# Performance work log

Hardware: AMD Instinct MI355X
Metric: run time of the kernel (lower is better)

The kernel has to match this reference:

```python
import jax, jax.numpy as jnp
import numpy as np

B, N, D, H = 2, 4096, 512, 8
HD = D // H


def setup_inputs() -> dict:
    key = jax.random.key(0)
    k1, k2, k3, k4, k5 = jax.random.split(key, 5)
    s = D ** -0.5  # init scale to keep activations sane
    return {
        "x": jax.random.normal(k1, (B, N, D), dtype=jnp.float32),
        "Wq": jax.random.normal(k2, (D, D), dtype=jnp.float32) * s,
        "bq": jax.random.normal(k3, (D,), dtype=jnp.float32) * 0.01,
        "Wk": jax.random.normal(k4, (D, D), dtype=jnp.float32) * s,
        "bk": jax.random.normal(k5, (D,), dtype=jnp.float32) * 0.01,
    }


def reference(x, Wq, bq, Wk, bk):
    b, n, d = x.shape
    # Linear layers: y = x @ W^T + b (torch convention: W is [out, in])
    q = (jnp.einsum("bnd,ed->bne", x, Wq) + bq).reshape(b, n, H, HD).transpose(0, 2, 1, 3)
    k = (jnp.einsum("bnd,ed->bne", x, Wk) + bk).reshape(b, n, H, HD).transpose(0, 2, 1, 3)
    # FAITHFUL BUG: original uses self.k(x) for v as well
    v = k
    # FAITHFUL QUIRK: scale by full dim D, not head_dim
    scale = d ** -0.5
    attn = jnp.einsum("bhqe,bhke->bhqk", q, k) * scale  # [B,H,N,N] materialized, as in original
    attn = jax.nn.softmax(attn, axis=-1)
    out = jnp.einsum("bhqk,bhke->bhqe", attn, v)  # [B,H,N,HD]
    return out.transpose(0, 2, 1, 3).reshape(b, n, d)
```

## Files before the change

### kernel.cpp

```cpp
#include <hip/hip_runtime.h>

#define B_  2
#define N_  4096
#define D_  512
#define H_  8
#define HD_ 64
#define SCL2 (0.04419417382415922f * 1.4426950408889634f)

typedef float  f32x4  __attribute__((ext_vector_type(4)));
typedef float  f32x16 __attribute__((ext_vector_type(16)));
typedef short  s16x8  __attribute__((ext_vector_type(8)));
typedef short  s16x4  __attribute__((ext_vector_type(4)));
typedef unsigned int u32x4 __attribute__((ext_vector_type(4)));

#define MFMA16(a,b,c) __builtin_amdgcn_mfma_f32_16x16x32_bf16((a),(b),(c),0,0,0)
#define MFMA32(a,b,c) __builtin_amdgcn_mfma_f32_32x32x16_bf16((a),(b),(c),0,0,0)

__device__ __forceinline__ unsigned bf16rtn(float x){
    unsigned u = __float_as_uint(x);
    return (u + 0x7FFFu + ((u >> 16) & 1u)) >> 16;
}
__device__ __forceinline__ float bf16tof(unsigned h){
    return __uint_as_float(h << 16);
}
__device__ __forceinline__ unsigned cvt_pk_bf16(float lo, float hi){
    unsigned r;
    asm("v_cvt_pk_bf16_f32 %0, %1, %2" : "=v"(r) : "v"(lo), "v"(hi));
    return r;
}
__device__ __forceinline__ void perm32swap(unsigned &a, unsigned &b){
    asm volatile("v_permlane32_swap_b32 %0, %1" : "+v"(a), "+v"(b));
}
__device__ __forceinline__ int ix16(int r, int c){
    return (r << 6) + ((((c >> 3) ^ (r & 7)) << 3) | (c & 7));
}
__device__ __forceinline__ int ixt(int r, int c){
    return (r << 6) + ((((c >> 3) ^ (r & 7) ^ ((r >> 3) & 7)) << 3) | (c & 7));
}

__global__ __launch_bounds__(256) void split_kernel(
    const float* __restrict__ x, const float* __restrict__ Wq, const float* __restrict__ Wk,
    short* __restrict__ xh, short* __restrict__ xl,
    short* __restrict__ wqh, short* __restrict__ wql,
    short* __restrict__ wkh, short* __restrict__ wkl)
{
    const int bid = blockIdx.x;
    const float* src; short* dh; short* dl; size_t base;
    if (bid < 2048)      { src = x;  dh = xh;  dl = xl;  base = (size_t)bid * 2048; }
    else if (bid < 2176) { src = Wq; dh = wqh; dl = wql; base = (size_t)(bid - 2048) * 2048; }
    else                 { src = Wk; dh = wkh; dl = wkl; base = (size_t)(bid - 2176) * 2048; }

    const size_t off = base + (size_t)threadIdx.x * 8;
    float4 a = *(const float4*)&src[off];
    float4 c = *(const float4*)&src[off + 4];
    float v[8] = {a.x,a.y,a.z,a.w, c.x,c.y,c.z,c.w};
    s16x8 oh, ol;
    #pragma unroll
    for (int j = 0; j < 8; ++j) {
        unsigned hh = bf16rtn(v[j]);
        float lo = v[j] - bf16tof(hh);
        unsigned ll = bf16rtn(lo);
        oh[j] = (short)hh; ol[j] = (short)ll;
    }
    *(s16x8*)&dh[off] = oh;
    *(s16x8*)&dl[off] = ol;
}

__global__ __launch_bounds__(256, 2) void proj_gemm(
    const short* __restrict__ xh, const short* __restrict__ xl,
    const short* __restrict__ wqh, const short* __restrict__ wql,
    const short* __restrict__ wkh, const short* __restrict__ wkl,
    const float* __restrict__ bq, const float* __restrict__ bk,
    float* __restrict__ Qout, short* __restrict__ Khi, short* __restrict__ Klo)
{
    __shared__ short Ah[8192], Al[8192], Bh[8192], Bl[8192];

    const short* gWh  = blockIdx.z ? wkh : wqh;
    const short* gWl  = blockIdx.z ? wkl : wql;
    const float* bias = blockIdx.z ? bk  : bq;

    const int m0 = blockIdx.x * 128;
    const int e0 = blockIdx.y * 128;
    const int tid = threadIdx.x;
    const int wave = tid >> 6, lane = tid & 63;
    const int lr = lane & 15, lg = lane >> 4;

    int srow[4], scol[4];
    #pragma unroll
    for (int s = 0; s < 4; ++s) {
        int slot = s * 256 + tid;
        srow[s] = slot >> 3;
        scol[s] = (slot & 7) << 3;
    }

    f32x4 acc[2][8] = {};
    s16x8 pah[4], pal[4], pbh[4], pbl[4];

    #pragma unroll
    for (int s = 0; s < 4; ++s) {
        size_t ao = (size_t)(m0 + srow[s]) * D_ + scol[s];
        size_t bo = (size_t)(e0 + srow[s]) * D_ + scol[s];
        pah[s] = *(const s16x8*)&xh[ao];  pal[s] = *(const s16x8*)&xl[ao];
        pbh[s] = *(const s16x8*)&gWh[bo]; pbl[s] = *(const s16x8*)&gWl[bo];
    }

    for (int kt = 0; kt < 8; ++kt) {
        if (kt) __syncthreads();
        #pragma unroll
        for (int s = 0; s < 4; ++s) {
            int d = ix16(srow[s], scol[s]);
            *(s16x8*)&Ah[d] = pah[s];  *(s16x8*)&Al[d] = pal[s];
            *(s16x8*)&Bh[d] = pbh[s];  *(s16x8*)&Bl[d] = pbl[s];
        }
        __syncthreads();
        if (kt < 7) {
            const int k0 = (kt + 1) * 64;
            #pragma unroll
            for (int s = 0; s < 4; ++s) {
                size_t ao = (size_t)(m0 + srow[s]) * D_ + k0 + scol[s];
                size_t bo = (size_t)(e0 + srow[s]) * D_ + k0 + scol[s];
                pah[s] = *(const s16x8*)&xh[ao];  pal[s] = *(const s16x8*)&xl[ao];
                pbh[s] = *(const s16x8*)&gWh[bo]; pbl[s] = *(const s16x8*)&gWl[bo];
            }
        }
        __builtin_amdgcn_s_setprio(1);
        #pragma unroll
        for (int ks = 0; ks < 2; ++ks) {
            s16x8 afh[2], afl[2];
            #pragma unroll
            for (int f = 0; f < 2; ++f) {
                int a = ix16(wave*32 + f*16 + lr, ks*32 + lg*8);
                afh[f] = *(const s16x8*)&Ah[a];
                afl[f] = *(const s16x8*)&Al[a];
            }
            #pragma unroll
            for (int t = 0; t < 8; ++t) {
                int bA = ix16(t*16 + lr, ks*32 + lg*8);
                s16x8 bfh = *(const s16x8*)&Bh[bA];
                s16x8 bfl = *(const s16x8*)&Bl[bA];
                #pragma unroll
                for (int f = 0; f < 2; ++f) {
                    acc[f][t] = MFMA16(afh[f], bfh, acc[f][t]);
                    acc[f][t] = MFMA16(afh[f], bfl, acc[f][t]);
                    acc[f][t] = MFMA16(afl[f], bfh, acc[f][t]);
                }
            }
        }
        __builtin_amdgcn_s_setprio(0);
    }

    float bb[8];
    #pragma unroll
    for (int t = 0; t < 8; ++t) bb[t] = bias[e0 + t*16 + lr];

    if (blockIdx.z == 0) {
        #pragma unroll
        for (int f = 0; f < 2; ++f)
            #pragma unroll
            for (int t = 0; t < 8; ++t)
                #pragma unroll
                for (int r = 0; r < 4; ++r) {
                    int row = m0 + wave*32 + f*16 + lg*4 + r;
                    Qout[(size_t)row * D_ + e0 + t*16 + lr] = acc[f][t][r] + bb[t];
                }
    } else {
        #pragma unroll
        for (int f = 0; f < 2; ++f)
            #pragma unroll
            for (int t = 0; t < 8; ++t)
                #pragma unroll
                for (int r = 0; r < 4; ++r) {
                    int row = m0 + wave*32 + f*16 + lg*4 + r;
                    float v = acc[f][t][r] + bb[t];
                    unsigned hh = bf16rtn(v);
                    float lo = v - bf16tof(hh);
                    unsigned ll = bf16rtn(lo);
                    size_t o = (size_t)row * D_ + e0 + t*16 + lr;
                    Khi[o] = (short)hh;
                    Klo[o] = (short)ll;
                }
    }
}

__global__ __launch_bounds__(256) void proj_kernel(
    const float* __restrict__ x,
    const float* __restrict__ Wq, const float* __restrict__ bq,
    const float* __restrict__ Wk, const float* __restrict__ bk,
    float* __restrict__ Qout, short* __restrict__ Khi, short* __restrict__ Klo)
{
    const float* W    = blockIdx.z ? Wk : Wq;
    const float* bias = blockIdx.z ? bk : bq;

    const int m0 = blockIdx.x * 128;
    const int e0 = blockIdx.y * 128;

    __shared__ float Xs[128][36];
    __shared__ float Ws[128 * 36];

    const int tid = threadIdx.x;
    const int tx = tid & 15, ty = tid >> 4;

    float acc[8][8] = {};

    for (int k0 = 0; k0 < D_; k0 += 32) {
        #pragma unroll
        for (int s = 0; s < 4; ++s) {
            int slot = s * 256 + tid;
            int r  = slot >> 3;
            int c4 = (slot & 7) << 2;
            *(float4*)&Xs[r][c4] = *(const float4*)&x[(size_t)(m0 + r) * D_ + k0 + c4];
            int wblk = ((c4 >> 2) ^ (r >> 3)) & 7;
            *(float4*)&Ws[r * 36 + wblk * 4] = *(const float4*)&W[(size_t)(e0 + r) * D_ + k0 + c4];
        }
        __syncthreads();
        #pragma unroll
        for (int k = 0; k < 32; k += 4) {
            float4 xa[8], wb[8];
            #pragma unroll
            for (int i = 0; i < 8; ++i) xa[i] = *(float4*)&Xs[ty*8+i][k];
            #pragma unroll
            for (int j = 0; j < 8; ++j) {
                int row = tx*8 + j;
                int blk = ((k >> 2) ^ (row >> 3)) & 7;
                wb[j] = *(float4*)&Ws[row * 36 + blk * 4];
            }
            #pragma unroll
            for (int i = 0; i < 8; ++i)
                #pragma unroll
                for (int j = 0; j < 8; ++j)
                    acc[i][j] += xa[i].x*wb[j].x + xa[i].y*wb[j].y
                               + xa[i].z*wb[j].z + xa[i].w*wb[j].w;
        }
        __syncthreads();
    }

    const float4 bv0 = *(const float4*)&bias[e0 + tx*8];
    const float4 bv1 = *(const float4*)&bias[e0 + tx*8 + 4];
    const float bj[8] = {bv0.x,bv0.y,bv0.z,bv0.w, bv1.x,bv1.y,bv1.z,bv1.w};

    if (blockIdx.z == 0) {
        #pragma unroll
        for (int i = 0; i < 8; ++i) {
            float o[8];
            #pragma unroll
            for (int j = 0; j < 8; ++j) o[j] = acc[i][j] + bj[j];
            size_t off = (size_t)(m0 + ty*8 + i) * D_ + e0 + tx*8;
            *(float4*)&Qout[off]     = *(float4*)&o[0];
            *(float4*)&Qout[off + 4] = *(float4*)&o[4];
        }
    } else {
        #pragma unroll
        for (int i = 0; i < 8; ++i) {
            s16x8 oh, ol;
            #pragma unroll
            for (int j = 0; j < 8; ++j) {
                float v = acc[i][j] + bj[j];
                unsigned hh = bf16rtn(v);
                float lo = v - bf16tof(hh);
                unsigned ll = bf16rtn(lo);
                oh[j] = (short)hh; ol[j] = (short)ll;
            }
            size_t off = (size_t)(m0 + ty*8 + i) * D_ + e0 + tx*8;
            *(s16x8*)&Khi[off] = oh;
            *(s16x8*)&Klo[off] = ol;
        }
    }
}

__global__ __launch_bounds__(256, 2) void attn_kernel(
    const float* __restrict__ Q,
    const short* __restrict__ Khi, const short* __restrict__ Klo,
    float* __restrict__ out)
{
    __shared__ __align__(16) char smem[32768];
    short* Khs  = (short*)smem;
    short* Kls  = Khs + 4096;
    short* Kths = Kls + 4096;
    short* Ktls = Kths + 4096;

    const int bid = blockIdx.x;
    const int xcd = bid & 7, kk = bid >> 3;
    const int bh  = (xcd << 1) | (kk >> 5);
    const int qt  = kk & 31;
    const int b = bh >> 3, h = bh & 7;
    const int q0 = qt * 128;

    const int tid  = threadIdx.x;
    const int wave = tid >> 6, lane = tid & 63;
    const int lq   = lane & 31;
    const int hi   = lane >> 5;

    s16x8 qbh[4], qbl[4];
    {
        const int qrow = q0 + wave*32 + lq;
        const float* qp = Q + ((size_t)(b*N_ + qrow)) * D_ + h*HD_ + hi*8;
        #pragma unroll
        for (int s = 0; s < 4; ++s) {
            float4 a = *(const float4*)(qp + s*16);
            float4 c = *(const float4*)(qp + s*16 + 4);
            float v[8] = {a.x,a.y,a.z,a.w,c.x,c.y,c.z,c.w};
            #pragma unroll
            for (int j = 0; j < 8; ++j) {
                float xv = v[j] * SCL2;
                unsigned hh = bf16rtn(xv);
                float lo = xv - bf16tof(hh);
                qbh[s][j] = (short)hh;
                qbl[s][j] = (short)bf16rtn(lo);
            }
        }
    }

    f32x16 oacc[2] = {};
    float mrun = -1e30f, lrun = 0.f;

    const int br = tid >> 4, bc = tid & 15;
    s16x4 rh[4], rl[4];

    {
        const size_t kbase = ((size_t)(b*N_ + br*4)) * D_ + h*HD_ + bc*4;
        #pragma unroll
        for (int i = 0; i < 4; ++i) {
            rh[i] = *(const s16x4*)&Khi[kbase + (size_t)i * D_];
            rl[i] = *(const s16x4*)&Klo[kbase + (size_t)i * D_];
        }
    }

    for (int kt = 0; kt < 64; ++kt) {
        #pragma unroll
        for (int i = 0; i < 4; ++i) {
            *(s16x4*)&Khs[ix16(br*4+i, bc*4)] = rh[i];
            *(s16x4*)&Kls[ix16(br*4+i, bc*4)] = rl[i];
        }
        #pragma unroll
        for (int j = 0; j < 4; ++j) {
            s16x4 th = { rh[0][j], rh[1][j], rh[2][j], rh[3][j] };
            s16x4 tl = { rl[0][j], rl[1][j], rl[2][j], rl[3][j] };
            *(s16x4*)&Kths[ixt(bc*4+j, br*4)] = th;
            *(s16x4*)&Ktls[ixt(bc*4+j, br*4)] = tl;
        }
        __syncthreads();

        if (kt < 63) {
            const size_t kbase = ((size_t)(b*N_ + (kt+1)*64 + br*4)) * D_ + h*HD_ + bc*4;
            #pragma unroll
            for (int i = 0; i < 4; ++i) {
                rh[i] = *(const s16x4*)&Khi[kbase + (size_t)i * D_];
                rl[i] = *(const s16x4*)&Klo[kbase + (size_t)i * D_];
            }
        }

        f32x16 sacc[2] = {};
        __builtin_amdgcn_s_setprio(1);
        #pragma unroll
        for (int t = 0; t < 2; ++t) {
            #pragma unroll
            for (int s = 0; s < 4; ++s) {
                s16x8 ah = *(const s16x8*)&Khs[ix16(t*32 + lq, s*16 + hi*8)];
                s16x8 al = *(const s16x8*)&Kls[ix16(t*32 + lq, s*16 + hi*8)];
                sacc[t] = MFMA32(ah, qbh[s], sacc[t]);
                sacc[t] = MFMA32(ah, qbl[s], sacc[t]);
                sacc[t] = MFMA32(al, qbh[s], sacc[t]);
            }
        }
        __builtin_amdgcn_s_setprio(0);

        float tr[16];
        #pragma unroll
        for (int r = 0; r < 16; ++r) tr[r] = fmaxf(sacc[0][r], sacc[1][r]);
        #pragma unroll
        for (int st = 8; st >= 1; st >>= 1)
            #pragma unroll
            for (int r = 0; r < st; ++r) tr[r] = fmaxf(tr[r], tr[r + st]);
        float mt = fmaxf(tr[0], __shfl_xor(tr[0], 32));
        const float mn  = fmaxf(mrun, mt);
        const float al_ = __builtin_amdgcn_exp2f(mrun - mn);
        mrun = mn;

        f32x16 p[2];
        #pragma unroll
        for (int t = 0; t < 2; ++t)
            #pragma unroll
            for (int r = 0; r < 16; ++r)
                p[t][r] = __builtin_amdgcn_exp2f(sacc[t][r] - mn);
        #pragma unroll
        for (int r = 0; r < 16; ++r) tr[r] = p[0][r] + p[1][r];
        #pragma unroll
        for (int st = 8; st >= 1; st >>= 1)
            #pragma unroll
            for (int r = 0; r < st; ++r) tr[r] += tr[r + st];
        float rs = tr[0] + __shfl_xor(tr[0], 32);
        lrun = lrun * al_ + rs;
        #pragma unroll
        for (int dt = 0; dt < 2; ++dt)
            #pragma unroll
            for (int r = 0; r < 16; ++r)
                oacc[dt][r] *= al_;

        __builtin_amdgcn_s_setprio(1);
        #pragma unroll
        for (int s = 0; s < 4; ++s) {
            const int tt = s >> 1, r0 = (s & 1) * 8;
            float ph[8], pl[8];
            #pragma unroll
            for (int j = 0; j < 8; ++j) {
                float pv = p[tt][r0 + j];
                float hf = __uint_as_float(__float_as_uint(pv) & 0xFFFF0000u);
                ph[j] = hf;
                pl[j] = pv - hf;
            }
            unsigned h0 = cvt_pk_bf16(ph[0], ph[1]);
            unsigned h1 = cvt_pk_bf16(ph[4], ph[5]);
            perm32swap(h0, h1);
            unsigned h2 = cvt_pk_bf16(ph[2], ph[3]);
            unsigned h3 = cvt_pk_bf16(ph[6], ph[7]);
            perm32swap(h2, h3);
            u32x4 wph = { h0, h2, h1, h3 };
            s16x8 pfh = __builtin_bit_cast(s16x8, wph);

            unsigned l0 = cvt_pk_bf16(pl[0], pl[1]);
            unsigned l1 = cvt_pk_bf16(pl[4], pl[5]);
            perm32swap(l0, l1);
            unsigned l2 = cvt_pk_bf16(pl[2], pl[3]);
            unsigned l3 = cvt_pk_bf16(pl[6], pl[7]);
            perm32swap(l2, l3);
            u32x4 wpl = { l0, l2, l1, l3 };
            s16x8 pfl = __builtin_bit_cast(s16x8, wpl);

            #pragma unroll
            for (int dt = 0; dt < 2; ++dt) {
                s16x8 vh = *(const s16x8*)&Kths[ixt(dt*32 + lq, s*16 + hi*8)];
                s16x8 vl = *(const s16x8*)&Ktls[ixt(dt*32 + lq, s*16 + hi*8)];
                oacc[dt] = MFMA32(vh, pfh, oacc[dt]);
                oacc[dt] = MFMA32(vl, pfh, oacc[dt]);
                oacc[dt] = MFMA32(vh, pfl, oacc[dt]);
            }
        }
        __builtin_amdgcn_s_setprio(0);
        __syncthreads();
    }

    const float inv = 1.0f / lrun;
    float* Os = (float*)smem;
    #pragma unroll
    for (int dt = 0; dt < 2; ++dt)
        #pragma unroll
        for (int g = 0; g < 4; ++g) {
            f32x4 w;
            #pragma unroll
            for (int e = 0; e < 4; ++e)
                w[e] = oacc[dt][g*4 + e] * inv;
            const int q = wave*32 + lq;
            const int dbase = dt*32 + g*8 + hi*4;
            *(f32x4*)&Os[q*64 + (dbase ^ (q & 28))] = w;
        }
    __syncthreads();
    #pragma unroll
    for (int rep = 0; rep < 8; ++rep) {
        const int row = (tid >> 4) + rep*16;
        const int c4  = (tid & 15) * 4;
        f32x4 w = *(const f32x4*)&Os[row*64 + (c4 ^ (row & 28))];
        *(f32x4*)&out[((size_t)(b*N_ + q0 + row)) * D_ + h*HD_ + c4] = w;
    }
}

extern "C" void kernel_launch(void* const* d_in, const int* in_sizes, int n_in,
                              void* d_out, int out_size, void* d_ws, size_t ws_size,
                              hipStream_t stream)
{
    const float* x  = (const float*)d_in[0];
    const float* Wq = (const float*)d_in[1];
    const float* bq = (const float*)d_in[2];
    const float* Wk = (const float*)d_in[3];
    const float* bk = (const float*)d_in[4];
    float* outp = (float*)d_out;

    char* wsb = (char*)d_ws;
    float* Qw  = (float*)wsb;
    short* Khi = (short*)(wsb + 16777216);
    short* Klo = Khi + 4194304;

    if (ws_size >= 52428800) {
        short* xh  = (short*)(wsb + 33554432);
        short* xl  = xh + 4194304;
        short* wqh = (short*)(wsb + 50331648);
        short* wql = wqh + 262144;
        short* wkh = wql + 262144;
        short* wkl = wkh + 262144;

        split_kernel<<<dim3(2304), dim3(256), 0, stream>>>(
            x, Wq, Wk, xh, xl, wqh, wql, wkh, wkl);
        proj_gemm<<<dim3(64, 4, 2), dim3(256), 0, stream>>>(
            xh, xl, wqh, wql, wkh, wkl, bq, bk, Qw, Khi, Klo);
    } else {
        dim3 gp(64, 4, 2);
        proj_kernel<<<gp, dim3(256), 0, stream>>>(x, Wq, bq, Wk, bk, Qw, Khi, Klo);
    }

    attn_kernel<<<dim3(512), dim3(256), 0, stream>>>(Qw, Khi, Klo, outp);
}
```

Baseline: 317.7 us.

## Split attention KV range across blocks with merge kernel and lazy rescaling

Shrinks attention blocks to 128 threads over 64 query rows and splits the key range into two halves per query tile, so 2048 blocks run instead of 512. A new merge kernel then combines the partial outputs using their saved max and sum values. The online-softmax rescale is skipped unless the running max grows by more than 8 (log2 units), which removes per-tile multiplies on the output accumulators. The cost is writing and re-reading partial outputs through workspace plus an extra launch, and the workspace reuses the region that holds the split-x buffers.

Measured after the change: 384.9 us. +21.1%, slower.

```diff
diff --git a/kernel.cpp b/kernel.cpp
--- a/kernel.cpp
+++ b/kernel.cpp
@@ -267,10 +267,11 @@
     }
 }
 
-__global__ __launch_bounds__(256, 2) void attn_kernel(
+template<int SPLIT>
+__global__ __launch_bounds__(128, 4) void attn_kernel(
     const float* __restrict__ Q,
     const short* __restrict__ Khi, const short* __restrict__ Klo,
-    float* __restrict__ out)
+    float* __restrict__ out, float* __restrict__ Opart, float* __restrict__ Ml)
 {
     __shared__ __align__(16) char smem[32768];
     short* Khs  = (short*)smem;
@@ -279,11 +280,26 @@
     short* Ktls = Kths + 4096;
 
     const int bid = blockIdx.x;
-    const int xcd = bid & 7, kk = bid >> 3;
-    const int bh  = (xcd << 1) | (kk >> 5);
-    const int qt  = kk & 31;
+    const int xcd = bid & 7;
+    int bh, qt, ks, pidx;
+    if (SPLIT) {
+        const int idx = bid >> 3;
+        bh = (xcd << 1) | (idx >> 7);
+        const int rem = idx & 127;
+        qt = rem >> 1;
+        ks = rem & 1;
+        pidx = (bh * 64 + qt) * 2 + ks;
+    } else {
+        const int idx = bid >> 3;
+        bh = (xcd << 1) | (idx >> 6);
+        qt = idx & 63;
+        ks = 0;
+        pidx = 0;
+    }
     const int b = bh >> 3, h = bh & 7;
-    const int q0 = qt * 128;
+    const int q0 = qt * 64;
+    const int kt0 = SPLIT ? ks * 32 : 0;
+    const int nkt = SPLIT ? 32 : 64;
 
     const int tid  = threadIdx.x;
     const int wave = tid >> 6, lane = tid & 63;
@@ -314,36 +330,39 @@
     float mrun = -1e30f, lrun = 0.f;
 
     const int br = tid >> 4, bc = tid & 15;
-    s16x4 rh[4], rl[4];
+    s16x4 rh[8], rl[8];
 
     {
-        const size_t kbase = ((size_t)(b*N_ + br*4)) * D_ + h*HD_ + bc*4;
-        #pragma unroll
-        for (int i = 0; i < 4; ++i) {
+        const size_t kbase = ((size_t)(b*N_ + kt0*64 + br*8)) * D_ + h*HD_ + bc*4;
+        #pragma unroll
+        for (int i = 0; i < 8; ++i) {
             rh[i] = *(const s16x4*)&Khi[kbase + (size_t)i * D_];
             rl[i] = *(const s16x4*)&Klo[kbase + (size_t)i * D_];
         }
     }
 
-    for (int kt = 0; kt < 64; ++kt) {
-        #pragma unroll
-        for (int i = 0; i < 4; ++i) {
-            *(s16x4*)&Khs[ix16(br*4+i, bc*4)] = rh[i];
-            *(s16x4*)&Kls[ix16(br*4+i, bc*4)] = rl[i];
-        }
-        #pragma unroll
-        for (int j = 0; j < 4; ++j) {
-            s16x4 th = { rh[0][j], rh[1][j], rh[2][j], rh[3][j] };
-            s16x4 tl = { rl[0][j], rl[1][j], rl[2][j], rl[3][j] };
-            *(s16x4*)&Kths[ixt(bc*4+j, br*4)] = th;
-            *(s16x4*)&Ktls[ixt(bc*4+j, br*4)] = tl;
-        }
-        __syncthreads();
-
-        if (kt < 63) {
-            const size_t kbase = ((size_t)(b*N_ + (kt+1)*64 + br*4)) * D_ + h*HD_ + bc*4;
-            #pragma unroll
-            for (int i = 0; i < 4; ++i) {
+    for (int it = 0; it < nkt; ++it) {
+        const int kt = kt0 + it;
+        #pragma unroll
+        for (int i = 0; i < 8; ++i) {
+            *(s16x4*)&Khs[ix16(br*8+i, bc*4)] = rh[i];
+            *(s16x4*)&Kls[ix16(br*8+i, bc*4)] = rl[i];
+        }
+        #pragma unroll
+        for (int half = 0; half < 2; ++half)
+            #pragma unroll
+            for (int j = 0; j < 4; ++j) {
+                s16x4 th = { rh[half*4+0][j], rh[half*4+1][j], rh[half*4+2][j], rh[half*4+3][j] };
+                s16x4 tl = { rl[half*4+0][j], rl[half*4+1][j], rl[half*4+2][j], rl[half*4+3][j] };
+                *(s16x4*)&Kths[ixt(bc*4+j, br*8 + half*4)] = th;
+                *(s16x4*)&Ktls[ixt(bc*4+j, br*8 + half*4)] = tl;
+            }
+        __syncthreads();
+
+        if (it < nkt - 1) {
+            const size_t kbase = ((size_t)(b*N_ + (kt+1)*64 + br*8)) * D_ + h*HD_ + bc*4;
+            #pragma unroll
+            for (int i = 0; i < 8; ++i) {
                 rh[i] = *(const s16x4*)&Khi[kbase + (size_t)i * D_];
                 rl[i] = *(const s16x4*)&Klo[kbase + (size_t)i * D_];
             }
@@ -372,29 +391,31 @@
             #pragma unroll
             for (int r = 0; r < st; ++r) tr[r] = fmaxf(tr[r], tr[r + st]);
         float mt = fmaxf(tr[0], __shfl_xor(tr[0], 32));
-        const float mn  = fmaxf(mrun, mt);
-        const float al_ = __builtin_amdgcn_exp2f(mrun - mn);
-        mrun = mn;
+        if (__any(mt > mrun + 8.0f)) {
+            const float mn  = fmaxf(mrun, mt);
+            const float al_ = __builtin_amdgcn_exp2f(mrun - mn);
+            mrun = mn;
+            lrun *= al_;
+            #pragma unroll
+            for (int dt = 0; dt < 2; ++dt)
+                #pragma unroll
+                for (int r = 0; r < 16; ++r)
+                    oacc[dt][r] *= al_;
+        }
 
         f32x16 p[2];
         #pragma unroll
         for (int t = 0; t < 2; ++t)
             #pragma unroll
             for (int r = 0; r < 16; ++r)
-                p[t][r] = __builtin_amdgcn_exp2f(sacc[t][r] - mn);
+                p[t][r] = __builtin_amdgcn_exp2f(sacc[t][r] - mrun);
         #pragma unroll
         for (int r = 0; r < 16; ++r) tr[r] = p[0][r] + p[1][r];
         #pragma unroll
         for (int st = 8; st >= 1; st >>= 1)
             #pragma unroll
             for (int r = 0; r < st; ++r) tr[r] += tr[r + st];
-        float rs = tr[0] + __shfl_xor(tr[0], 32);
-        lrun = lrun * al_ + rs;
-        #pragma unroll
-        for (int dt = 0; dt < 2; ++dt)
-            #pragma unroll
-            for (int r = 0; r < 16; ++r)
-                oacc[dt][r] *= al_;
+        lrun += tr[0] + __shfl_xor(tr[0], 32);
 
         __builtin_amdgcn_s_setprio(1);
         #pragma unroll
@@ -439,27 +460,86 @@
         __syncthreads();
     }
 
-    const float inv = 1.0f / lrun;
-    float* Os = (float*)smem;
+    if (SPLIT) {
+        float* Op = Opart + (size_t)pidx * 4096;
+        #pragma unroll
+        for (int dt = 0; dt < 2; ++dt)
+            #pragma unroll
+            for (int r = 0; r < 16; ++r) {
+                const int d = dt*32 + (r & 3) + 8*(r >> 2) + 4*hi;
+                Op[d*64 + wave*32 + lq] = oacc[dt][r];
+            }
+        if (hi == 0) {
+            Ml[(size_t)pidx*128 + wave*32 + lq]      = mrun;
+            Ml[(size_t)pidx*128 + 64 + wave*32 + lq] = lrun;
+        }
+    } else {
+        const float inv = 1.0f / lrun;
+        float* Os = (float*)smem;
+        __syncthreads();
+        #pragma unroll
+        for (int dt = 0; dt < 2; ++dt)
+            #pragma unroll
+            for (int g = 0; g < 4; ++g) {
+                f32x4 w;
+                #pragma unroll
+                for (int e = 0; e < 4; ++e)
+                    w[e] = oacc[dt][g*4 + e] * inv;
+                const int q = wave*32 + lq;
+                const int dbase = dt*32 + g*8 + hi*4;
+                *(f32x4*)&Os[q*64 + (dbase ^ (q & 28))] = w;
+            }
+        __syncthreads();
+        #pragma unroll
+        for (int rep = 0; rep < 8; ++rep) {
+            const int row = (tid >> 4) + rep*8;
+            const int c4  = (tid & 15) * 4;
+            f32x4 w = *(const f32x4*)&Os[row*64 + (c4 ^ (row & 28))];
+            *(f32x4*)&out[((size_t)(b*N_ + q0 + row)) * D_ + h*HD_ + c4] = w;
+        }
+    }
+}
+
+__global__ __launch_bounds__(256) void merge_kernel(
+    const float* __restrict__ Opart, const float* __restrict__ Ml,
+    float* __restrict__ out)
+{
+    const int bid = blockIdx.x;
+    const int bh = bid >> 6, qt = bid & 63;
+    const int b = bh >> 3, h = bh & 7;
+    const int q0 = qt * 64;
+    const int p0 = bid * 2, p1 = bid * 2 + 1;
+
+    const int tid = threadIdx.x;
+    const int tq = tid & 63, dg = tid >> 6;
+
+    const float m1 = Ml[(size_t)p0*128 + tq], l1 = Ml[(size_t)p0*128 + 64 + tq];
+    const float m2 = Ml[(size_t)p1*128 + tq], l2 = Ml[(size_t)p1*128 + 64 + tq];
+    const float m  = fmaxf(m1, m2);
+    const float s1 = __builtin_amdgcn_exp2f(m1 - m);
+    const float s2 = __builtin_amdgcn_exp2f(m2 - m);
+    const float linv = 1.0f / (l1*s1 + l2*s2);
+
+    __shared__ float T[64 * 65];
+    const float* O1 = Opart + (size_t)p0 * 4096;
+    const float* O2 = Opart + (size_t)p1 * 4096;
     #pragma unroll
-    for (int dt = 0; dt < 2; ++dt)
-        #pragma unroll
-        for (int g = 0; g < 4; ++g) {
-            f32x4 w;
-            #pragma unroll
-            for (int e = 0; e < 4; ++e)
-                w[e] = oacc[dt][g*4 + e] * inv;
-            const int q = wave*32 + lq;
-            const int dbase = dt*32 + g*8 + hi*4;
-            *(f32x4*)&Os[q*64 + (dbase ^ (q & 28))] = w;
-        }
+    for (int i = 0; i < 16; ++i) {
+        const int d = dg*16 + i;
+        const float v = (O1[d*64 + tq]*s1 + O2[d*64 + tq]*s2) * linv;
+        T[tq*65 + d] = v;
+    }
     __syncthreads();
+
+    const int row = tid >> 2;
+    const int c0  = (tid & 3) * 16;
     #pragma unroll
-    for (int rep = 0; rep < 8; ++rep) {
-        const int row = (tid >> 4) + rep*16;
-        const int c4  = (tid & 15) * 4;
-        f32x4 w = *(const f32x4*)&Os[row*64 + (c4 ^ (row & 28))];
-        *(f32x4*)&out[((size_t)(b*N_ + q0 + row)) * D_ + h*HD_ + c4] = w;
+    for (int g = 0; g < 4; ++g) {
+        f32x4 w;
+        #pragma unroll
+        for (int e = 0; e < 4; ++e)
+            w[e] = T[row*65 + c0 + g*4 + e];
+        *(f32x4*)&out[((size_t)(b*N_ + q0 + row)) * D_ + h*HD_ + c0 + g*4] = w;
     }
 }
 
@@ -496,5 +576,14 @@
         proj_kernel<<<gp, dim3(256), 0, stream>>>(x, Wq, bq, Wk, bk, Qw, Khi, Klo);
     }
 
-    attn_kernel<<<dim3(512), dim3(256), 0, stream>>>(Qw, Khi, Klo, outp);
-}
+    if (ws_size >= 68157440) {
+        float* Opart = (float*)(wsb + 33554432);
+        float* Ml    = (float*)(wsb + 67108864);
+        attn_kernel<1><<<dim3(2048), dim3(128), 0, stream>>>(
+            Qw, Khi, Klo, outp, Opart, Ml);
+        merge_kernel<<<dim3(1024), dim3(256), 0, stream>>>(Opart, Ml, outp);
+    } else {
+        attn_kernel<0><<<dim3(1024), dim3(128), 0, stream>>>(
+            Qw, Khi, Klo, outp, nullptr, nullptr);
+    }
+}
```

## Double K tile to 128 rows and add lazy softmax rescaling

Applied to the files above, without the earlier changes.

The attention kernel now stages 128 keys per iteration instead of 64, which doubles shared memory to 64KB and halves the number of loop iterations and barriers. A new swizzle handles the wider transposed K tile. The online softmax now skips rescaling the running max, sum and output accumulator unless some lane's tile max exceeds the running max by more than 8 in log2 units. This trades fewer rescale multiplies for more registers per thread and the LDS occupancy limit implied by 64KB per block with launch_bounds(256,2).

After: 291.8 us. -8.1%, faster.

```diff
diff --git a/kernel.cpp b/kernel.cpp
--- a/kernel.cpp
+++ b/kernel.cpp
@@ -34,8 +34,8 @@
 __device__ __forceinline__ int ix16(int r, int c){
     return (r << 6) + ((((c >> 3) ^ (r & 7)) << 3) | (c & 7));
 }
-__device__ __forceinline__ int ixt(int r, int c){
-    return (r << 6) + ((((c >> 3) ^ (r & 7) ^ ((r >> 3) & 7)) << 3) | (c & 7));
+__device__ __forceinline__ int ixt2(int r, int c){
+    return (r << 7) + ((((c >> 3) ^ ((r >> 2) & 15)) << 3) | (c & 7));
 }
 
 __global__ __launch_bounds__(256) void split_kernel(
@@ -272,11 +272,11 @@
     const short* __restrict__ Khi, const short* __restrict__ Klo,
     float* __restrict__ out)
 {
-    __shared__ __align__(16) char smem[32768];
+    __shared__ __align__(16) char smem[65536];
     short* Khs  = (short*)smem;
-    short* Kls  = Khs + 4096;
-    short* Kths = Kls + 4096;
-    short* Ktls = Kths + 4096;
+    short* Kls  = Khs + 8192;
+    short* Kths = Kls + 8192;
+    short* Ktls = Kths + 8192;
 
     const int bid = blockIdx.x;
     const int xcd = bid & 7, kk = bid >> 3;
@@ -313,46 +313,47 @@
     f32x16 oacc[2] = {};
     float mrun = -1e30f, lrun = 0.f;
 
-    const int br = tid >> 4, bc = tid & 15;
-    s16x4 rh[4], rl[4];
+    const int rg = tid >> 4, bc = tid & 15;
+    s16x4 rh[8], rl[8];
 
     {
-        const size_t kbase = ((size_t)(b*N_ + br*4)) * D_ + h*HD_ + bc*4;
-        #pragma unroll
-        for (int i = 0; i < 4; ++i) {
+        const size_t kbase = ((size_t)(b*N_ + rg*8)) * D_ + h*HD_ + bc*4;
+        #pragma unroll
+        for (int i = 0; i < 8; ++i) {
             rh[i] = *(const s16x4*)&Khi[kbase + (size_t)i * D_];
             rl[i] = *(const s16x4*)&Klo[kbase + (size_t)i * D_];
         }
     }
 
-    for (int kt = 0; kt < 64; ++kt) {
-        #pragma unroll
-        for (int i = 0; i < 4; ++i) {
-            *(s16x4*)&Khs[ix16(br*4+i, bc*4)] = rh[i];
-            *(s16x4*)&Kls[ix16(br*4+i, bc*4)] = rl[i];
+    for (int kt = 0; kt < 32; ++kt) {
+        #pragma unroll
+        for (int i = 0; i < 8; ++i) {
+            *(s16x4*)&Khs[ix16(rg*8+i, bc*4)] = rh[i];
+            *(s16x4*)&Kls[ix16(rg*8+i, bc*4)] = rl[i];
         }
         #pragma unroll
         for (int j = 0; j < 4; ++j) {
-            s16x4 th = { rh[0][j], rh[1][j], rh[2][j], rh[3][j] };
-            s16x4 tl = { rl[0][j], rl[1][j], rl[2][j], rl[3][j] };
-            *(s16x4*)&Kths[ixt(bc*4+j, br*4)] = th;
-            *(s16x4*)&Ktls[ixt(bc*4+j, br*4)] = tl;
+            s16x8 th, tl;
+            #pragma unroll
+            for (int i = 0; i < 8; ++i) { th[i] = rh[i][j]; tl[i] = rl[i][j]; }
+            *(s16x8*)&Kths[ixt2(bc*4+j, rg*8)] = th;
+            *(s16x8*)&Ktls[ixt2(bc*4+j, rg*8)] = tl;
         }
         __syncthreads();
 
-        if (kt < 63) {
-            const size_t kbase = ((size_t)(b*N_ + (kt+1)*64 + br*4)) * D_ + h*HD_ + bc*4;
-            #pragma unroll
-            for (int i = 0; i < 4; ++i) {
+        if (kt < 31) {
+            const size_t kbase = ((size_t)(b*N_ + (kt+1)*128 + rg*8)) * D_ + h*HD_ + bc*4;
+            #pragma unroll
+            for (int i = 0; i < 8; ++i) {
                 rh[i] = *(const s16x4*)&Khi[kbase + (size_t)i * D_];
                 rl[i] = *(const s16x4*)&Klo[kbase + (size_t)i * D_];
             }
         }
 
-        f32x16 sacc[2] = {};
+        f32x16 sacc[4] = {};
         __builtin_amdgcn_s_setprio(1);
         #pragma unroll
-        for (int t = 0; t < 2; ++t) {
+        for (int t = 0; t < 4; ++t) {
             #pragma unroll
             for (int s = 0; s < 4; ++s) {
                 s16x8 ah = *(const s16x8*)&Khs[ix16(t*32 + lq, s*16 + hi*8)];
@@ -366,39 +367,44 @@
 
         float tr[16];
         #pragma unroll
-        for (int r = 0; r < 16; ++r) tr[r] = fmaxf(sacc[0][r], sacc[1][r]);
+        for (int r = 0; r < 16; ++r)
+            tr[r] = fmaxf(fmaxf(sacc[0][r], sacc[1][r]),
+                          fmaxf(sacc[2][r], sacc[3][r]));
         #pragma unroll
         for (int st = 8; st >= 1; st >>= 1)
             #pragma unroll
             for (int r = 0; r < st; ++r) tr[r] = fmaxf(tr[r], tr[r + st]);
         float mt = fmaxf(tr[0], __shfl_xor(tr[0], 32));
-        const float mn  = fmaxf(mrun, mt);
-        const float al_ = __builtin_amdgcn_exp2f(mrun - mn);
-        mrun = mn;
-
-        f32x16 p[2];
-        #pragma unroll
-        for (int t = 0; t < 2; ++t)
+        if (__any(mt > mrun + 8.0f)) {
+            const float mn  = fmaxf(mrun, mt);
+            const float al_ = __builtin_amdgcn_exp2f(mrun - mn);
+            mrun = mn;
+            lrun *= al_;
+            #pragma unroll
+            for (int dt = 0; dt < 2; ++dt)
+                #pragma unroll
+                for (int r = 0; r < 16; ++r)
+                    oacc[dt][r] *= al_;
+        }
+
+        f32x16 p[4];
+        #pragma unroll
+        for (int t = 0; t < 4; ++t)
             #pragma unroll
             for (int r = 0; r < 16; ++r)
-                p[t][r] = __builtin_amdgcn_exp2f(sacc[t][r] - mn);
-        #pragma unroll
-        for (int r = 0; r < 16; ++r) tr[r] = p[0][r] + p[1][r];
+                p[t][r] = __builtin_amdgcn_exp2f(sacc[t][r] - mrun);
+        #pragma unroll
+        for (int r = 0; r < 16; ++r)
+            tr[r] = (p[0][r] + p[1][r]) + (p[2][r] + p[3][r]);
         #pragma unroll
         for (int st = 8; st >= 1; st >>= 1)
             #pragma unroll
             for (int r = 0; r < st; ++r) tr[r] += tr[r + st];
-        float rs = tr[0] + __shfl_xor(tr[0], 32);
-        lrun = lrun * al_ + rs;
-        #pragma unroll
-        for (int dt = 0; dt < 2; ++dt)
-            #pragma unroll
-            for (int r = 0; r < 16; ++r)
-                oacc[dt][r] *= al_;
+        lrun += tr[0] + __shfl_xor(tr[0], 32);
 
         __builtin_amdgcn_s_setprio(1);
         #pragma unroll
-        for (int s = 0; s < 4; ++s) {
+        for (int s = 0; s < 8; ++s) {
             const int tt = s >> 1, r0 = (s & 1) * 8;
             float ph[8], pl[8];
             #pragma unroll
@@ -428,8 +434,8 @@
 
             #pragma unroll
             for (int dt = 0; dt < 2; ++dt) {
-                s16x8 vh = *(const s16x8*)&Kths[ixt(dt*32 + lq, s*16 + hi*8)];
-                s16x8 vl = *(const s16x8*)&Ktls[ixt(dt*32 + lq, s*16 + hi*8)];
+                s16x8 vh = *(const s16x8*)&Kths[ixt2(dt*32 + lq, s*16 + hi*8)];
+                s16x8 vl = *(const s16x8*)&Ktls[ixt2(dt*32 + lq, s*16 + hi*8)];
                 oacc[dt] = MFMA32(vh, pfh, oacc[dt]);
                 oacc[dt] = MFMA32(vl, pfh, oacc[dt]);
                 oacc[dt] = MFMA32(vh, pfl, oacc[dt]);
```
